# Performance work log

Measured on AMD Instinct MI355X. Metric: run time of the kernel, lower is better.

Reference implementation:

```python
import jax, jax.numpy as jnp
import numpy as np

B, T, D_MODEL, NHEAD, D_HEAD = 8, 4096, 1024, 16, 64


def setup_inputs() -> dict:
    key = jax.random.key(0)
    ks = jax.random.split(key, 8)
    return {
        "inputs": jax.random.normal(ks[0], (B, T, D_MODEL), jnp.float32),
        "z0": jax.random.normal(ks[1], (NHEAD, D_HEAD), jnp.float32),
        "W_in": jax.random.normal(ks[2], (D_MODEL, D_MODEL), jnp.float32) / np.sqrt(D_MODEL),
        "b_in": jax.random.normal(ks[3], (D_MODEL,), jnp.float32) * 0.01,
        "W_out": jax.random.normal(ks[4], (D_MODEL, D_MODEL), jnp.float32) / np.sqrt(D_MODEL),
        "b_out": jax.random.normal(ks[5], (D_MODEL,), jnp.float32) * 0.01,
        "smoothing_logit": jax.random.normal(ks[6], (NHEAD, 1), jnp.float32),
        "v0": jax.random.normal(ks[7], (1, 1, NHEAD, D_HEAD), jnp.float32),
    }


def reference(inputs, z0, W_in, b_in, W_out, b_out, smoothing_logit, v0):
    b, t, d = inputs.shape
    nhead, d_head = z0.shape
    # in projection -> (b, t, h, d_head)
    values = (inputs @ W_in + b_in).reshape(b, t, nhead, d_head)
    # prepend learned z0, then temporal differencing -> (b, t, h, d_head)
    z0_b = jnp.broadcast_to(z0[None, None], (b, 1, nhead, d_head))
    values = jnp.concatenate([z0_b, values], axis=1)
    values = values[:, 1:] - values[:, :-1]
    # exponential smoothing recurrence: s_j = a*s_{j-1} + (1-a)*v_j, s_{-1} = v0
    alpha = jax.nn.sigmoid(smoothing_logit)           # (h, 1)
    a = alpha[None]                                   # (1, h, 1) broadcast over batch
    s0 = jnp.broadcast_to(v0[0, 0][None], (b, nhead, d_head))

    def step(s, v):                                   # v: (b, h, d_head)
        s = a * s + (1.0 - a) * v
        return s, s

    _, es_out = jax.lax.scan(step, s0, jnp.swapaxes(values, 0, 1))  # (t, b, h, d)
    es_out = jnp.swapaxes(es_out, 0, 1)               # (b, t, h, d_head)
    # prepend v0 -> length t+1
    v0_b = jnp.broadcast_to(v0, (b, 1, nhead, d_head))
    out = jnp.concatenate([v0_b, es_out], axis=1)     # (b, t+1, h, d_head)
    out = out.reshape(b, t + 1, nhead * d_head)
    return out @ W_out + b_out                        # (b, t+1, d_model)
```

## Files before the change

### kernel.cpp

```cpp
#include <hip/hip_runtime.h>
#include <hip/hip_bf16.h>
#include <stdint.h>

#define DEV static __device__ __forceinline__

typedef __attribute__((ext_vector_type(8))) short bf16x8;
typedef __attribute__((ext_vector_type(4))) float f32x4;
typedef unsigned int u32;

static constexpr int T = 4096;
static constexpr int BATCH = 8;
static constexpr int DM = 1024;
static constexpr int M1 = BATCH * T;
static constexpr int M2 = BATCH * (T + 1);
static constexpr int M2P = 129 * 256;
static constexpr int NCH = 64;
static constexpr int CL = T / NCH;
static constexpr int NT = 32;

DEV unsigned short f2bf(float f) {
  union { float f; unsigned u; } v; v.f = f;
  unsigned u = v.u;
  return (unsigned short)((u + 0x7fffu + ((u >> 16) & 1u)) >> 16);
}
DEV float bf2f(unsigned short s) {
  union { unsigned u; float f; } v; v.u = ((unsigned)s) << 16;
  return v.f;
}

DEV void gl_lds16(const unsigned short* g, unsigned short* lds) {
  __builtin_amdgcn_global_load_lds(
      (const __attribute__((address_space(1))) u32*)g,
      (__attribute__((address_space(3))) u32*)lds,
      16, 0, 0);
}

DEV bf16x8 ds_read128(unsigned byte_off) {
  bf16x8 r;
  asm volatile("ds_read_b128 %0, %1" : "=v"(r) : "v"(byte_off));
  return r;
}

__global__ void k_cvt_x(const float4* __restrict__ x, ushort4* __restrict__ o) {
  int i = blockIdx.x * 256 + threadIdx.x;
  float4 v = x[i];
  ushort4 r;
  r.x = f2bf(v.x); r.y = f2bf(v.y); r.z = f2bf(v.z); r.w = f2bf(v.w);
  o[i] = r;
}

__global__ void k_transpose(const float* __restrict__ w0, const float* __restrict__ w1,
                            unsigned short* __restrict__ t0, unsigned short* __restrict__ t1) {
  __shared__ float tile[32][33];
  const float* src = blockIdx.z ? w1 : w0;
  unsigned short* dst = blockIdx.z ? t1 : t0;
  int bx = blockIdx.x * 32;
  int by = blockIdx.y * 32;
  int tx = threadIdx.x & 31, ty = threadIdx.x >> 5;
#pragma unroll
  for (int r = 0; r < 32; r += 8)
    tile[ty + r][tx] = src[(by + ty + r) * DM + bx + tx];
  __syncthreads();
#pragma unroll
  for (int r = 0; r < 32; r += 8)
    dst[(bx + ty + r) * DM + by + tx] = f2bf(tile[tx][ty + r]);
}

template <int MODE>
__global__ __launch_bounds__(512, 2) void k_gemm(const unsigned short* __restrict__ A16,
                                                 const unsigned short* __restrict__ Bt16,
                                                 const float* __restrict__ bias,
                                                 unsigned short* __restrict__ outb,
                                                 float* __restrict__ outf, int Mvalid) {
  __shared__ unsigned short lds[4 * 16384];

  const int tid = threadIdx.x;
  const int w = tid >> 6, l = tid & 63;
  const int wm = w >> 2, wn = w & 3;
  const int rr = l & 15, kg = l >> 4;

  const int nwg = gridDim.x, orig = blockIdx.x;
  const int q = nwg >> 3, r8 = nwg & 7;
  const int xcd = orig & 7, idx = orig >> 3;
  const int wg = (xcd < r8 ? xcd * (q + 1) : r8 * (q + 1) + (xcd - r8) * q) + idx;
  const int bm = wg >> 2, bn = wg & 3;
  const int blockM = bm * 256;
  const int blockN = bn * 256;

  f32x4 acc[8][4];
#pragma unroll
  for (int m = 0; m < 8; m++)
#pragma unroll
    for (int n = 0; n < 4; n++) acc[m][n] = (f32x4){0.f, 0.f, 0.f, 0.f};

  const unsigned short* pA[2];
  const unsigned short* pB[2];
#pragma unroll
  for (int cc = 0; cc < 2; cc++) {
    int rp = w * 32 + cc * 16 + (l >> 2);
    int sl = (l & 3) ^ ((rp >> 1) & 3);
    pA[cc] = A16 + (size_t)(blockM + rp) * DM + sl * 8;
    pB[cc] = Bt16 + (size_t)(blockN + rp) * DM + sl * 8;
  }

  const unsigned ldsbase =
      (unsigned)(size_t)(__attribute__((address_space(3))) unsigned short*)lds;
  unsigned offA[8], offB[4];
#pragma unroll
  for (int mf = 0; mf < 8; mf++) {
    int rrow = wm * 128 + mf * 16 + rr;
    offA[mf] = ldsbase + rrow * 64 + ((kg ^ ((rrow >> 1) & 3)) * 16);
  }
#pragma unroll
  for (int nf = 0; nf < 4; nf++) {
    int rb = wn * 64 + nf * 16 + rr;
    offB[nf] = ldsbase + 16384 + rb * 64 + ((kg ^ ((rb >> 1) & 3)) * 16);
  }

  auto stageA = [&](int t) {
    unsigned short* d = lds + (t & 3) * 16384 + w * 1024;
#pragma unroll
    for (int cc = 0; cc < 2; cc++) gl_lds16(pA[cc] + (size_t)t * 32, d + cc * 512);
  };
  auto stageB = [&](int t) {
    unsigned short* d = lds + (t & 3) * 16384 + 8192 + w * 1024;
#pragma unroll
    for (int cc = 0; cc < 2; cc++) gl_lds16(pB[cc] + (size_t)t * 32, d + cc * 512);
  };

  stageA(0); stageB(0);
  stageA(1); stageB(1);
  stageA(2); stageB(2);

  for (int t = 0; t < NT; ++t) {
    if (t < NT - 2)       asm volatile("s_waitcnt vmcnt(8)" ::: "memory");
    else if (t == NT - 2) asm volatile("s_waitcnt vmcnt(4)" ::: "memory");
    else                  asm volatile("s_waitcnt vmcnt(0)" ::: "memory");
    __builtin_amdgcn_s_barrier();

    const unsigned bufoff = (unsigned)((t & 3) * 32768);
    const bool do_stage = (t + 3 < NT);

    bf16x8 bq[4], aq[4];
#pragma unroll
    for (int nf = 0; nf < 4; nf++) bq[nf] = ds_read128(bufoff + offB[nf]);
#pragma unroll
    for (int mf = 0; mf < 4; mf++) aq[mf] = ds_read128(bufoff + offA[mf]);
    if (do_stage) stageA(t + 3);
    asm volatile("s_waitcnt lgkmcnt(0)" ::: "memory");
    __builtin_amdgcn_sched_barrier(0);
    __builtin_amdgcn_s_setprio(1);
#pragma unroll
    for (int mf = 0; mf < 4; mf++)
#pragma unroll
      for (int nf = 0; nf < 4; nf++)
        acc[mf][nf] = __builtin_amdgcn_mfma_f32_16x16x32_bf16(aq[mf], bq[nf], acc[mf][nf], 0, 0, 0);
    __builtin_amdgcn_s_setprio(0);
    __builtin_amdgcn_s_barrier();

#pragma unroll
    for (int mf = 0; mf < 4; mf++) aq[mf] = ds_read128(bufoff + offA[4 + mf]);
    if (do_stage) stageB(t + 3);
    asm volatile("s_waitcnt lgkmcnt(0)" ::: "memory");
    __builtin_amdgcn_sched_barrier(0);
    __builtin_amdgcn_s_setprio(1);
#pragma unroll
    for (int mf = 0; mf < 4; mf++)
#pragma unroll
      for (int nf = 0; nf < 4; nf++)
        acc[4 + mf][nf] = __builtin_amdgcn_mfma_f32_16x16x32_bf16(aq[mf], bq[nf], acc[4 + mf][nf], 0, 0, 0);
    __builtin_amdgcn_s_setprio(0);
  }

#pragma unroll
  for (int nf = 0; nf < 4; nf++) {
    int col = blockN + wn * 64 + nf * 16 + (l & 15);
    float bv = bias[col];
#pragma unroll
    for (int mf = 0; mf < 8; mf++) {
      int row = blockM + wm * 128 + mf * 16 + (l >> 4) * 4;
#pragma unroll
      for (int j = 0; j < 4; j++) {
        float v = acc[mf][nf][j] + bv;
        if (MODE == 0) {
          outb[(size_t)(row + j) * DM + col] = f2bf(v);
        } else {
          if (row + j < Mvalid) outf[(size_t)(row + j) * DM + col] = v;
        }
      }
    }
  }
}

__global__ void k_scan_partial(const unsigned short* __restrict__ proj,
                               const float* __restrict__ logit,
                               const float* __restrict__ z0,
                               float* __restrict__ chunkend) {
  int b = blockIdx.x >> 6, c = blockIdx.x & 63;
  int ch = threadIdx.x;
  float a = 1.f / (1.f + expf(-logit[ch >> 6]));
  int t0 = c * CL;
  const unsigned short* p = proj + (size_t)(b * T + t0) * DM + ch;
  float pprev = (t0 == 0) ? z0[ch] : bf2f(p[-DM]);
  float s = 0.f;
  for (int j = 0; j < CL; j++) {
    float pv = bf2f(p[(size_t)j * DM]);
    s = a * s + (1.f - a) * (pv - pprev);
    pprev = pv;
  }
  chunkend[(b * NCH + c) * DM + ch] = s;
}

__global__ void k_scan_combine(const float* __restrict__ chunkend,
                               const float* __restrict__ logit,
                               const float* __restrict__ v0,
                               float* __restrict__ enter) {
  int b = blockIdx.x;
  int ch = threadIdx.x;
  float a = 1.f / (1.f + expf(-logit[ch >> 6]));
  float a2 = a * a, a4 = a2 * a2, a8 = a4 * a4, a16 = a8 * a8, a32 = a16 * a16;
  float aL = a32 * a32;
  float e = v0[ch];
  enter[(b * NCH + 0) * DM + ch] = e;
  for (int c = 1; c < NCH; c++) {
    e = aL * e + chunkend[(b * NCH + c - 1) * DM + ch];
    enter[(b * NCH + c) * DM + ch] = e;
  }
}

__global__ void k_scan_final(const unsigned short* __restrict__ proj,
                             const float* __restrict__ logit,
                             const float* __restrict__ z0,
                             const float* __restrict__ v0,
                             const float* __restrict__ enter,
                             unsigned short* __restrict__ S) {
  int b = blockIdx.x >> 6, c = blockIdx.x & 63;
  int ch = threadIdx.x;
  float a = 1.f / (1.f + expf(-logit[ch >> 6]));
  int t0 = c * CL;
  const unsigned short* p = proj + (size_t)(b * T + t0) * DM + ch;
  unsigned short* so = S + (size_t)(b * (T + 1) + t0 + 1) * DM + ch;
  float pprev = (t0 == 0) ? z0[ch] : bf2f(p[-DM]);
  float s = enter[(b * NCH + c) * DM + ch];
  if (c == 0) S[(size_t)b * (T + 1) * DM + ch] = f2bf(v0[ch]);
  for (int j = 0; j < CL; j++) {
    float pv = bf2f(p[(size_t)j * DM]);
    s = a * s + (1.f - a) * (pv - pprev);
    pprev = pv;
    so[(size_t)j * DM] = f2bf(s);
  }
}

__global__ void k_pad(unsigned short* __restrict__ S) {
  int i = blockIdx.x * 256 + threadIdx.x;
  if (i < (M2P - M2) * DM) S[(size_t)M2 * DM + i] = 0;
}

extern "C" void kernel_launch(void* const* d_in, const int* in_sizes, int n_in,
                              void* d_out, int out_size, void* d_ws, size_t ws_size,
                              hipStream_t stream) {
  const float* inputs = (const float*)d_in[0];
  const float* z0     = (const float*)d_in[1];
  const float* W_in   = (const float*)d_in[2];
  const float* b_in   = (const float*)d_in[3];
  const float* W_out  = (const float*)d_in[4];
  const float* b_out  = (const float*)d_in[5];
  const float* slogit = (const float*)d_in[6];
  const float* v0     = (const float*)d_in[7];
  float* out = (float*)d_out;

  char* ws = (char*)d_ws;
  unsigned short* X16   = (unsigned short*)(ws);
  unsigned short* P16   = (unsigned short*)(ws + 67108864);
  unsigned short* S16   = (unsigned short*)(ws + 134217728);
  unsigned short* WTin  = (unsigned short*)(ws + 201850880);
  unsigned short* WTout = (unsigned short*)(ws + 203948032);
  float* chunkend       = (float*)(ws + 206045184);
  float* enter          = (float*)(ws + 208142336);

  k_cvt_x<<<32768, 256, 0, stream>>>((const float4*)inputs, (ushort4*)X16);
  k_transpose<<<dim3(32, 32, 2), 256, 0, stream>>>(W_in, W_out, WTin, WTout);
  k_gemm<0><<<dim3((M1 / 256) * 4), 512, 0, stream>>>(X16, WTin, b_in, P16, nullptr, M1);
  k_scan_partial<<<dim3(BATCH * NCH), 1024, 0, stream>>>(P16, slogit, z0, chunkend);
  k_scan_combine<<<dim3(BATCH), 1024, 0, stream>>>(chunkend, slogit, v0, enter);
  k_scan_final<<<dim3(BATCH * NCH), 1024, 0, stream>>>(P16, slogit, z0, v0, enter, S16);
  k_pad<<<dim3(992), 256, 0, stream>>>(S16);
  k_gemm<1><<<dim3((M2P / 256) * 4), 512, 0, stream>>>(S16, WTout, b_out, nullptr, out, M2);
}
```

Baseline: 304.5 us.

## Use 64-wide K tiles with double-buffered LDS in bf16 GEMM

The GEMM main loop moves from 32-wide K tiles with a 4-stage ring buffer to 64-wide K tiles with two LDS buffers. The LDS layout becomes 128-byte rows with an XOR swizzle over 8 slots. Staging of the next tile is split across the sub-phases, so half of A is issued early and the rest of A plus all of B is issued late. This halves the number of loop iterations and barriers per tile, in exchange for shallower prefetch depth (two stages instead of three) and more live registers.

```diff
diff --git a/kernel.cpp b/kernel.cpp
--- a/kernel.cpp
+++ b/kernel.cpp
@@ -16,7 +16,7 @@
 static constexpr int M2P = 129 * 256;
 static constexpr int NCH = 64;
 static constexpr int CL = T / NCH;
-static constexpr int NT = 32;
+static constexpr int NT = 16;
 
 DEV unsigned short f2bf(float f) {
   union { float f; unsigned u; } v; v.f = f;
@@ -72,7 +72,7 @@
                                                  const float* __restrict__ bias,
                                                  unsigned short* __restrict__ outb,
                                                  float* __restrict__ outf, int Mvalid) {
-  __shared__ unsigned short lds[4 * 16384];
+  __shared__ unsigned short lds[2 * 32768];
 
   const int tid = threadIdx.x;
   const int w = tid >> 6, l = tid & 63;
@@ -80,9 +80,9 @@
   const int rr = l & 15, kg = l >> 4;
 
   const int nwg = gridDim.x, orig = blockIdx.x;
-  const int q = nwg >> 3, r8 = nwg & 7;
+  const int q8 = nwg >> 3, r8 = nwg & 7;
   const int xcd = orig & 7, idx = orig >> 3;
-  const int wg = (xcd < r8 ? xcd * (q + 1) : r8 * (q + 1) + (xcd - r8) * q) + idx;
+  const int wg = (xcd < r8 ? xcd * (q8 + 1) : r8 * (q8 + 1) + (xcd - r8) * q8) + idx;
   const int bm = wg >> 2, bn = wg & 3;
   const int blockM = bm * 256;
   const int blockN = bn * 256;
@@ -93,60 +93,52 @@
 #pragma unroll
     for (int n = 0; n < 4; n++) acc[m][n] = (f32x4){0.f, 0.f, 0.f, 0.f};
 
-  const unsigned short* pA[2];
-  const unsigned short* pB[2];
-#pragma unroll
-  for (int cc = 0; cc < 2; cc++) {
-    int rp = w * 32 + cc * 16 + (l >> 2);
-    int sl = (l & 3) ^ ((rp >> 1) & 3);
-    pA[cc] = A16 + (size_t)(blockM + rp) * DM + sl * 8;
-    pB[cc] = Bt16 + (size_t)(blockN + rp) * DM + sl * 8;
-  }
+  const int srow = w * 8 + (l >> 3);
+  const int sslot = (l & 7) ^ ((l >> 3) & 7);
+  const unsigned short* pA = A16 + (size_t)(blockM + srow) * DM + sslot * 8;
+  const unsigned short* pB = Bt16 + (size_t)(blockN + srow) * DM + sslot * 8;
+
+  auto stage = [&](int t, int q, bool isB) {
+    unsigned short* d = lds + (t & 1) * 32768 + (isB ? 16384 : 0) + q * 4096 + w * 512;
+    gl_lds16((isB ? pB : pA) + (size_t)q * 64 * DM + (size_t)t * 64, d);
+  };
 
   const unsigned ldsbase =
       (unsigned)(size_t)(__attribute__((address_space(3))) unsigned short*)lds;
-  unsigned offA[8], offB[4];
-#pragma unroll
-  for (int mf = 0; mf < 8; mf++) {
-    int rrow = wm * 128 + mf * 16 + rr;
-    offA[mf] = ldsbase + rrow * 64 + ((kg ^ ((rrow >> 1) & 3)) * 16);
-  }
-#pragma unroll
-  for (int nf = 0; nf < 4; nf++) {
-    int rb = wn * 64 + nf * 16 + rr;
-    offB[nf] = ldsbase + 16384 + rb * 64 + ((kg ^ ((rb >> 1) & 3)) * 16);
-  }
-
-  auto stageA = [&](int t) {
-    unsigned short* d = lds + (t & 3) * 16384 + w * 1024;
-#pragma unroll
-    for (int cc = 0; cc < 2; cc++) gl_lds16(pA[cc] + (size_t)t * 32, d + cc * 512);
-  };
-  auto stageB = [&](int t) {
-    unsigned short* d = lds + (t & 3) * 16384 + 8192 + w * 1024;
-#pragma unroll
-    for (int cc = 0; cc < 2; cc++) gl_lds16(pB[cc] + (size_t)t * 32, d + cc * 512);
-  };
-
-  stageA(0); stageB(0);
-  stageA(1); stageB(1);
-  stageA(2); stageB(2);
+  unsigned offA[2][8], offB[2][4];
+#pragma unroll
+  for (int h = 0; h < 2; h++) {
+#pragma unroll
+    for (int mf = 0; mf < 8; mf++) {
+      int r = wm * 128 + mf * 16 + rr;
+      offA[h][mf] = ldsbase + r * 128 + ((((h << 2) | kg) ^ (r & 7)) << 4);
+    }
+#pragma unroll
+    for (int nf = 0; nf < 4; nf++) {
+      int r = wn * 64 + nf * 16 + rr;
+      offB[h][nf] = ldsbase + 32768 + r * 128 + ((((h << 2) | kg) ^ (r & 7)) << 4);
+    }
+  }
+
+#pragma unroll
+  for (int q = 0; q < 4; q++) { stage(0, q, false); stage(0, q, true); }
+  stage(1, 0, false); stage(1, 2, false);
+#pragma unroll
+  for (int q = 0; q < 4; q++) stage(1, q, true);
 
   for (int t = 0; t < NT; ++t) {
-    if (t < NT - 2)       asm volatile("s_waitcnt vmcnt(8)" ::: "memory");
-    else if (t == NT - 2) asm volatile("s_waitcnt vmcnt(4)" ::: "memory");
-    else                  asm volatile("s_waitcnt vmcnt(0)" ::: "memory");
+    if (t < NT - 1) asm volatile("s_waitcnt vmcnt(6)" ::: "memory");
+    else            asm volatile("s_waitcnt vmcnt(0)" ::: "memory");
     __builtin_amdgcn_s_barrier();
 
-    const unsigned bufoff = (unsigned)((t & 3) * 32768);
-    const bool do_stage = (t + 3 < NT);
-
-    bf16x8 bq[4], aq[4];
-#pragma unroll
-    for (int nf = 0; nf < 4; nf++) bq[nf] = ds_read128(bufoff + offB[nf]);
-#pragma unroll
-    for (int mf = 0; mf < 4; mf++) aq[mf] = ds_read128(bufoff + offA[mf]);
-    if (do_stage) stageA(t + 3);
+    const unsigned bo = (unsigned)((t & 1) * 65536);
+    bf16x8 aq[4], bq0[4], bq1[4];
+
+#pragma unroll
+    for (int nf = 0; nf < 4; nf++) bq0[nf] = ds_read128(bo + offB[0][nf]);
+#pragma unroll
+    for (int mf = 0; mf < 4; mf++) aq[mf] = ds_read128(bo + offA[0][mf]);
+    if (t + 1 < NT) { stage(t + 1, 1, false); stage(t + 1, 3, false); }
     asm volatile("s_waitcnt lgkmcnt(0)" ::: "memory");
     __builtin_amdgcn_sched_barrier(0);
     __builtin_amdgcn_s_setprio(1);
@@ -154,13 +146,12 @@
     for (int mf = 0; mf < 4; mf++)
 #pragma unroll
       for (int nf = 0; nf < 4; nf++)
-        acc[mf][nf] = __builtin_amdgcn_mfma_f32_16x16x32_bf16(aq[mf], bq[nf], acc[mf][nf], 0, 0, 0);
+        acc[mf][nf] = __builtin_amdgcn_mfma_f32_16x16x32_bf16(aq[mf], bq0[nf], acc[mf][nf], 0, 0, 0);
     __builtin_amdgcn_s_setprio(0);
     __builtin_amdgcn_s_barrier();
 
 #pragma unroll
-    for (int mf = 0; mf < 4; mf++) aq[mf] = ds_read128(bufoff + offA[4 + mf]);
-    if (do_stage) stageB(t + 3);
+    for (int mf = 0; mf < 4; mf++) aq[mf] = ds_read128(bo + offA[0][4 + mf]);
     asm volatile("s_waitcnt lgkmcnt(0)" ::: "memory");
     __builtin_amdgcn_sched_barrier(0);
     __builtin_amdgcn_s_setprio(1);
@@ -168,7 +159,40 @@
     for (int mf = 0; mf < 4; mf++)
 #pragma unroll
       for (int nf = 0; nf < 4; nf++)
-        acc[4 + mf][nf] = __builtin_amdgcn_mfma_f32_16x16x32_bf16(aq[mf], bq[nf], acc[4 + mf][nf], 0, 0, 0);
+        acc[4 + mf][nf] = __builtin_amdgcn_mfma_f32_16x16x32_bf16(aq[mf], bq0[nf], acc[4 + mf][nf], 0, 0, 0);
+    __builtin_amdgcn_s_setprio(0);
+    __builtin_amdgcn_s_barrier();
+
+#pragma unroll
+    for (int nf = 0; nf < 4; nf++) bq1[nf] = ds_read128(bo + offB[1][nf]);
+#pragma unroll
+    for (int mf = 0; mf < 4; mf++) aq[mf] = ds_read128(bo + offA[1][mf]);
+    asm volatile("s_waitcnt lgkmcnt(0)" ::: "memory");
+    __builtin_amdgcn_sched_barrier(0);
+    __builtin_amdgcn_s_setprio(1);
+#pragma unroll
+    for (int mf = 0; mf < 4; mf++)
+#pragma unroll
+      for (int nf = 0; nf < 4; nf++)
+        acc[mf][nf] = __builtin_amdgcn_mfma_f32_16x16x32_bf16(aq[mf], bq1[nf], acc[mf][nf], 0, 0, 0);
+    __builtin_amdgcn_s_setprio(0);
+    __builtin_amdgcn_s_barrier();
+
+#pragma unroll
+    for (int mf = 0; mf < 4; mf++) aq[mf] = ds_read128(bo + offA[1][4 + mf]);
+    if (t + 2 < NT) {
+      stage(t + 2, 0, false); stage(t + 2, 2, false);
+#pragma unroll
+      for (int q = 0; q < 4; q++) stage(t + 2, q, true);
+    }
+    asm volatile("s_waitcnt lgkmcnt(0)" ::: "memory");
+    __builtin_amdgcn_sched_barrier(0);
+    __builtin_amdgcn_s_setprio(1);
+#pragma unroll
+    for (int mf = 0; mf < 4; mf++)
+#pragma unroll
+      for (int nf = 0; nf < 4; nf++)
+        acc[4 + mf][nf] = __builtin_amdgcn_mfma_f32_16x16x32_bf16(aq[mf], bq1[nf], acc[4 + mf][nf], 0, 0, 0);
     __builtin_amdgcn_s_setprio(0);
   }
 
```

Result: faster. 291.6 us (-4.2%).

## Restructure GEMM main loop into 8-phase ping-pong with BK=64 double buffer

Applied to the files above, without the earlier changes.

Rewrites the bf16 GEMM kernel's main loop to use a K-tile of 64 instead of 32, with two 64KB-slot LDS buffers split into A/B halves, so each iteration runs eight phases that each load part of the next tile while computing a 2x4 quadrant of fragments. The wave-to-tile mapping changes to a 4x2 arrangement with 32x64 per-wave sub-blocks in each quadrant, and the LDS swizzle becomes an 8-way XOR for 128-byte rows. This aims to hide global-to-LDS latency better and cut barrier overhead per unit of K work, at the cost of more barriers per tile and a more complex schedule with finer vmcnt accounting.

```diff
diff --git a/kernel.cpp b/kernel.cpp
--- a/kernel.cpp
+++ b/kernel.cpp
@@ -16,7 +16,7 @@
 static constexpr int M2P = 129 * 256;
 static constexpr int NCH = 64;
 static constexpr int CL = T / NCH;
-static constexpr int NT = 32;
+static constexpr int NT = 16;
 
 DEV unsigned short f2bf(float f) {
   union { float f; unsigned u; } v; v.f = f;
@@ -72,116 +72,119 @@
                                                  const float* __restrict__ bias,
                                                  unsigned short* __restrict__ outb,
                                                  float* __restrict__ outf, int Mvalid) {
-  __shared__ unsigned short lds[4 * 16384];
+  __shared__ unsigned short lds[65536];
 
   const int tid = threadIdx.x;
   const int w = tid >> 6, l = tid & 63;
-  const int wm = w >> 2, wn = w & 3;
+  const int wmm = w & 3, wn = w >> 2;
   const int rr = l & 15, kg = l >> 4;
 
   const int nwg = gridDim.x, orig = blockIdx.x;
-  const int q = nwg >> 3, r8 = nwg & 7;
+  const int q8 = nwg >> 3, r8 = nwg & 7;
   const int xcd = orig & 7, idx = orig >> 3;
-  const int wg = (xcd < r8 ? xcd * (q + 1) : r8 * (q + 1) + (xcd - r8) * q) + idx;
+  const int wg = (xcd < r8 ? xcd * (q8 + 1) : r8 * (q8 + 1) + (xcd - r8) * q8) + idx;
   const int bm = wg >> 2, bn = wg & 3;
   const int blockM = bm * 256;
   const int blockN = bn * 256;
 
-  f32x4 acc[8][4];
-#pragma unroll
-  for (int m = 0; m < 8; m++)
-#pragma unroll
-    for (int n = 0; n < 4; n++) acc[m][n] = (f32x4){0.f, 0.f, 0.f, 0.f};
-
+  f32x4 acc[4][8];
+#pragma unroll
+  for (int m = 0; m < 4; m++)
+#pragma unroll
+    for (int n = 0; n < 8; n++) acc[m][n] = (f32x4){0.f, 0.f, 0.f, 0.f};
+
+  const int sslot = (l & 7) ^ ((l >> 3) & 7);
   const unsigned short* pA[2];
   const unsigned short* pB[2];
 #pragma unroll
-  for (int cc = 0; cc < 2; cc++) {
-    int rp = w * 32 + cc * 16 + (l >> 2);
-    int sl = (l & 3) ^ ((rp >> 1) & 3);
-    pA[cc] = A16 + (size_t)(blockM + rp) * DM + sl * 8;
-    pB[cc] = Bt16 + (size_t)(blockN + rp) * DM + sl * 8;
-  }
+  for (int c = 0; c < 2; c++) {
+    int rp = (w * 2 + c) * 8 + (l >> 3);
+    pA[c] = A16 + (size_t)(blockM + rp) * DM + sslot * 8;
+    pB[c] = Bt16 + (size_t)(blockN + rp) * DM + sslot * 8;
+  }
+
+#define STAGE(tt, isB, H)                                                          \
+  do {                                                                             \
+    unsigned short* d_ = lds + ((tt) & 1) * 32768 + (isB) * 16384 + (H) * 8192 + w * 1024; \
+    gl_lds16(pA[0] + ((isB) ? (pB[0] - pA[0]) : 0) + (size_t)(H) * 128 * DM + (size_t)(tt) * 64, d_);       \
+    gl_lds16(pA[1] + ((isB) ? (pB[1] - pA[1]) : 0) + (size_t)(H) * 128 * DM + (size_t)(tt) * 64, d_ + 512); \
+  } while (0)
 
   const unsigned ldsbase =
       (unsigned)(size_t)(__attribute__((address_space(3))) unsigned short*)lds;
-  unsigned offA[8], offB[4];
-#pragma unroll
-  for (int mf = 0; mf < 8; mf++) {
-    int rrow = wm * 128 + mf * 16 + rr;
-    offA[mf] = ldsbase + rrow * 64 + ((kg ^ ((rrow >> 1) & 3)) * 16);
-  }
-#pragma unroll
-  for (int nf = 0; nf < 4; nf++) {
-    int rb = wn * 64 + nf * 16 + rr;
-    offB[nf] = ldsbase + 16384 + rb * 64 + ((kg ^ ((rb >> 1) & 3)) * 16);
-  }
-
-  auto stageA = [&](int t) {
-    unsigned short* d = lds + (t & 3) * 16384 + w * 1024;
-#pragma unroll
-    for (int cc = 0; cc < 2; cc++) gl_lds16(pA[cc] + (size_t)t * 32, d + cc * 512);
-  };
-  auto stageB = [&](int t) {
-    unsigned short* d = lds + (t & 3) * 16384 + 8192 + w * 1024;
-#pragma unroll
-    for (int cc = 0; cc < 2; cc++) gl_lds16(pB[cc] + (size_t)t * 32, d + cc * 512);
-  };
-
-  stageA(0); stageB(0);
-  stageA(1); stageB(1);
-  stageA(2); stageB(2);
-
-  for (int t = 0; t < NT; ++t) {
-    if (t < NT - 2)       asm volatile("s_waitcnt vmcnt(8)" ::: "memory");
-    else if (t == NT - 2) asm volatile("s_waitcnt vmcnt(4)" ::: "memory");
-    else                  asm volatile("s_waitcnt vmcnt(0)" ::: "memory");
-    __builtin_amdgcn_s_barrier();
-
-    const unsigned bufoff = (unsigned)((t & 3) * 32768);
-    const bool do_stage = (t + 3 < NT);
-
-    bf16x8 bq[4], aq[4];
-#pragma unroll
-    for (int nf = 0; nf < 4; nf++) bq[nf] = ds_read128(bufoff + offB[nf]);
-#pragma unroll
-    for (int mf = 0; mf < 4; mf++) aq[mf] = ds_read128(bufoff + offA[mf]);
-    if (do_stage) stageA(t + 3);
-    asm volatile("s_waitcnt lgkmcnt(0)" ::: "memory");
-    __builtin_amdgcn_sched_barrier(0);
-    __builtin_amdgcn_s_setprio(1);
-#pragma unroll
-    for (int mf = 0; mf < 4; mf++)
-#pragma unroll
-      for (int nf = 0; nf < 4; nf++)
-        acc[mf][nf] = __builtin_amdgcn_mfma_f32_16x16x32_bf16(aq[mf], bq[nf], acc[mf][nf], 0, 0, 0);
-    __builtin_amdgcn_s_setprio(0);
-    __builtin_amdgcn_s_barrier();
-
-#pragma unroll
-    for (int mf = 0; mf < 4; mf++) aq[mf] = ds_read128(bufoff + offA[4 + mf]);
-    if (do_stage) stageB(t + 3);
-    asm volatile("s_waitcnt lgkmcnt(0)" ::: "memory");
-    __builtin_amdgcn_sched_barrier(0);
-    __builtin_amdgcn_s_setprio(1);
-#pragma unroll
-    for (int mf = 0; mf < 4; mf++)
-#pragma unroll
-      for (int nf = 0; nf < 4; nf++)
-        acc[4 + mf][nf] = __builtin_amdgcn_mfma_f32_16x16x32_bf16(aq[mf], bq[nf], acc[4 + mf][nf], 0, 0, 0);
-    __builtin_amdgcn_s_setprio(0);
-  }
-
-#pragma unroll
-  for (int nf = 0; nf < 4; nf++) {
-    int col = blockN + wn * 64 + nf * 16 + (l & 15);
+  unsigned aoffv[2][2], boffv[4][2];
+#pragma unroll
+  for (int kh = 0; kh < 2; kh++) {
+    int g = kh * 4 + kg;
+#pragma unroll
+    for (int mf = 0; mf < 2; mf++) {
+      int r = wmm * 32 + mf * 16 + rr;
+      aoffv[mf][kh] = ldsbase + r * 128 + (((g) ^ (l & 7)) * 16);
+    }
+#pragma unroll
+    for (int nf = 0; nf < 4; nf++) {
+      int r = wn * 64 + nf * 16 + rr;
+      boffv[nf][kh] = ldsbase + r * 128 + (((g) ^ (l & 7)) * 16);
+    }
+  }
+
+#define PH(SLOT, A_, B_, STG, VMW)                                                     \
+  do {                                                                                 \
+    bf16x8 aq_[2][2], bq_[4][2];                                                       \
+    _Pragma("unroll") for (int kh = 0; kh < 2; kh++) {                                 \
+      _Pragma("unroll") for (int nf = 0; nf < 4; nf++)                                 \
+        bq_[nf][kh] = ds_read128(boffv[nf][kh] + ((SLOT) * 65536u + 32768u + (B_) * 16384u)); \
+      _Pragma("unroll") for (int mf = 0; mf < 2; mf++)                                 \
+        aq_[mf][kh] = ds_read128(aoffv[mf][kh] + ((SLOT) * 65536u + (A_) * 16384u));   \
+    }                                                                                  \
+    STG;                                                                               \
+    VMW;                                                                               \
+    __builtin_amdgcn_s_barrier();                                                      \
+    asm volatile("s_waitcnt lgkmcnt(0)" ::: "memory");                                 \
+    __builtin_amdgcn_sched_barrier(0);                                                 \
+    __builtin_amdgcn_s_setprio(1);                                                     \
+    _Pragma("unroll") for (int kh = 0; kh < 2; kh++)                                   \
+      _Pragma("unroll") for (int mf = 0; mf < 2; mf++)                                 \
+        _Pragma("unroll") for (int nf = 0; nf < 4; nf++)                               \
+          acc[(A_) * 2 + mf][(B_) * 4 + nf] = __builtin_amdgcn_mfma_f32_16x16x32_bf16( \
+              aq_[mf][kh], bq_[nf][kh], acc[(A_) * 2 + mf][(B_) * 4 + nf], 0, 0, 0);   \
+    __builtin_amdgcn_s_setprio(0);                                                     \
+    __builtin_amdgcn_s_barrier();                                                      \
+  } while (0)
+
+#define VM4 asm volatile("s_waitcnt vmcnt(4)" ::: "memory")
+#define VM0 asm volatile("s_waitcnt vmcnt(0)" ::: "memory")
+
+  STAGE(0, 0, 0); STAGE(0, 1, 0); STAGE(0, 0, 1); STAGE(0, 1, 1);
+  STAGE(1, 0, 0); STAGE(1, 1, 0);
+  VM4;
+  __builtin_amdgcn_s_barrier();
+
+  for (int i = 0; i < NT / 2; ++i) {
+    const int t0 = 2 * i;
+    const bool g1 = (t0 + 2 < NT), g2 = (t0 + 3 < NT);
+    PH(0, 0, 0, STAGE(t0 + 1, 0, 1), );
+    PH(0, 0, 1, STAGE(t0 + 1, 1, 1), );
+    PH(0, 1, 0, if (g1) STAGE(t0 + 2, 0, 0), );
+    PH(0, 1, 1, if (g1) STAGE(t0 + 2, 1, 0), if (g1) { VM4; } else { VM0; });
+    PH(1, 0, 0, if (g1) STAGE(t0 + 2, 0, 1), );
+    PH(1, 0, 1, if (g1) STAGE(t0 + 2, 1, 1), );
+    PH(1, 1, 0, if (g2) STAGE(t0 + 3, 0, 0), );
+    PH(1, 1, 1, if (g2) STAGE(t0 + 3, 1, 0), if (g2) { VM4; } else { VM0; });
+  }
+#undef PH
+#undef STAGE
+
+#pragma unroll
+  for (int N = 0; N < 8; N++) {
+    int col = blockN + (N >> 2) * 128 + wn * 64 + (N & 3) * 16 + (l & 15);
     float bv = bias[col];
 #pragma unroll
-    for (int mf = 0; mf < 8; mf++) {
-      int row = blockM + wm * 128 + mf * 16 + (l >> 4) * 4;
+    for (int M = 0; M < 4; M++) {
+      int row = blockM + (M >> 1) * 128 + wmm * 32 + (M & 1) * 16 + (l >> 4) * 4;
 #pragma unroll
       for (int j = 0; j < 4; j++) {
-        float v = acc[mf][nf][j] + bv;
+        float v = acc[M][N][j] + bv;
         if (MODE == 0) {
           outb[(size_t)(row + j) * DM + col] = f2bf(v);
         } else {
```

Measured after the change: 304.4 us. Within noise of the previous version (-0.0%).
